# Performance work log

Measured on AMD Instinct MI355X. Metric: run time of the kernel, lower is better.

Reference implementation:

```python
import jax, jax.numpy as jnp
import numpy as np

BATCH, SEQ, IN_DIM, OUT_DIM = 8, 512, 32, 1
D_MODEL, N_LAYERS = 512, 4
D_INNER = 2 * D_MODEL          # expand_factor=2
D_STATE = 16
D_CONV = 4
DT_RANK = (D_MODEL + 15) // 16  # ceil(d_model/16) = 32


def setup_inputs() -> dict:
    key = jax.random.key(0)
    ks = iter(jax.random.split(key, 24))
    def w(shape, fan_in):
        return jax.random.normal(next(ks), shape, jnp.float32) * (fan_in ** -0.5)
    dt = jax.random.uniform(next(ks), (N_LAYERS, D_INNER), jnp.float32, 1e-3, 0.1)
    A_log = jnp.broadcast_to(jnp.log(jnp.arange(1, D_STATE + 1, dtype=jnp.float32)),
                             (N_LAYERS, D_INNER, D_STATE)) * 1.0
    return {
        "x": jax.random.normal(next(ks), (BATCH, SEQ, IN_DIM), jnp.float32),
        "enc_w": w((D_MODEL, IN_DIM), IN_DIM),
        "enc_b": jnp.zeros((D_MODEL,), jnp.float32),
        "in_proj_w": w((N_LAYERS, 2 * D_INNER, D_MODEL), D_MODEL),
        "conv_w": w((N_LAYERS, D_INNER, 1, D_CONV), D_CONV),
        "conv_b": jnp.zeros((N_LAYERS, D_INNER), jnp.float32),
        "x_proj_w": w((N_LAYERS, DT_RANK + 2 * D_STATE, D_INNER), D_INNER),
        "dt_proj_w": w((N_LAYERS, D_INNER, DT_RANK), DT_RANK),
        "dt_proj_b": jnp.log(jnp.expm1(dt)),  # inverse softplus init
        "A_log": A_log,
        "D": jnp.ones((N_LAYERS, D_INNER), jnp.float32),
        "out_proj_w": w((N_LAYERS, D_MODEL, D_INNER), D_INNER),
        "norm_w": jnp.ones((N_LAYERS, D_MODEL), jnp.float32),
        "dec_w1": w((D_MODEL // 2, D_MODEL), D_MODEL),
        "dec_b1": jnp.zeros((D_MODEL // 2,), jnp.float32),
        "dec_w2": w((OUT_DIM, D_MODEL // 2), D_MODEL // 2),
        "dec_b2": jnp.zeros((OUT_DIM,), jnp.float32),
    }


def _rmsnorm(x, w, eps=1e-5):
    return x * jax.lax.rsqrt(jnp.mean(x * x, axis=-1, keepdims=True) + eps) * w


def _mixer(x, in_w, cw, cb, xp_w, dtp_w, dtp_b, A_log, Dp, out_w):
    B, L, _ = x.shape
    xz = x @ in_w.T                               # (B,L,2*di)
    xr, z = jnp.split(xz, 2, axis=-1)
    # causal depthwise conv1d (cross-correlation, left pad d_conv-1)
    xc = jax.lax.conv_general_dilated(
        xr.transpose(0, 2, 1), cw, window_strides=(1,),
        padding=[(D_CONV - 1, 0)], feature_group_count=D_INNER,
        dimension_numbers=("NCW", "OIW", "NCW"))    # (B,di,L)
    xr = jax.nn.silu(xc.transpose(0, 2, 1) + cb)   # (B,L,di)
    dbc = xr @ xp_w.T                              # (B,L,dt_rank+2N)
    delta = jax.nn.softplus(dbc[..., :DT_RANK] @ dtp_w.T + dtp_b)  # (B,L,di)
    Bm = dbc[..., DT_RANK:DT_RANK + D_STATE]       # (B,L,N)
    Cm = dbc[..., DT_RANK + D_STATE:]              # (B,L,N)
    A = -jnp.exp(A_log)                            # (di,N)
    dA = jnp.exp(delta[..., None] * A)             # (B,L,di,N)
    dBx = delta[..., None] * Bm[:, :, None, :] * xr[..., None]
    def step(h, inputs):
        dA_t, dBx_t = inputs
        h = dA_t * h + dBx_t
        return h, h
    h0 = jnp.zeros((B, D_INNER, D_STATE), xr.dtype)
    _, hs = jax.lax.scan(step, h0, (dA.transpose(1, 0, 2, 3), dBx.transpose(1, 0, 2, 3)))
    y = jnp.einsum("lbdn,bln->bld", hs, Cm) + Dp * xr
    y = y * jax.nn.silu(z)
    return y @ out_w.T


def reference(x, enc_w, enc_b, in_proj_w, conv_w, conv_b, x_proj_w, dt_proj_w,
              dt_proj_b, A_log, D, out_proj_w, norm_w, dec_w1, dec_b1, dec_w2, dec_b2):
    h = x @ enc_w.T + enc_b
    for i in range(in_proj_w.shape[0]):   # residual pre-norm Mamba blocks
        h = h + _mixer(_rmsnorm(h, norm_w[i]), in_proj_w[i], conv_w[i], conv_b[i],
                       x_proj_w[i], dt_proj_w[i], dt_proj_b[i], A_log[i], D[i],
                       out_proj_w[i])
    h = h[:, -1, :]
    h = jax.nn.relu(h @ dec_w1.T + dec_b1)
    return (h @ dec_w2.T + dec_b2).reshape(-1)
```

## Files before the change

### kernel.cpp

```cpp
#include <hip/hip_runtime.h>
#include <math.h>

#define BATCH   8
#define SEQ     512
#define IN_DIM  32
#define D_MODEL 512
#define N_LAYERS 4
#define D_INNER 1024
#define D_STATE 16
#define D_CONV  4
#define DT_RANK 32
#define NTOK    (BATCH * SEQ)
#define BLK_T   32
#define NCHUNK  (SEQ / BLK_T)

typedef __attribute__((ext_vector_type(8))) short short8_t;
typedef __attribute__((ext_vector_type(4))) float floatx4;

__device__ __forceinline__ float sigmoidf_(float x) { return 1.f / (1.f + __expf(-x)); }

__device__ __forceinline__ unsigned short f2bf(float f) {
    unsigned int u = __float_as_uint(f);
    return (unsigned short)((u + 0x7fffu + ((u >> 16) & 1u)) >> 16);
}
__device__ __forceinline__ float bf2f(unsigned short u) {
    return __uint_as_float((unsigned int)u << 16);
}

__global__ __launch_bounds__(256) void cast_all_kernel(
    const float* __restrict__ a, unsigned short* __restrict__ oa, int qa,
    const float* __restrict__ b, unsigned short* __restrict__ ob, int qb,
    const float* __restrict__ c, unsigned short* __restrict__ oc, int qc)
{
    int v = blockIdx.x * 256 + threadIdx.x;
    const float* in; unsigned short* out;
    if (v < qa)                { in = a; out = oa; }
    else if (v < qa + qb)      { v -= qa; in = b; out = ob; }
    else if (v < qa + qb + qc) { v -= qa + qb; in = c; out = oc; }
    else return;
    const float4 x = *(const float4*)&in[v * 4];
    ushort4 o;
    o.x = f2bf(x.x); o.y = f2bf(x.y); o.z = f2bf(x.z); o.w = f2bf(x.w);
    *(ushort4*)&out[v * 4] = o;
}

template<int BM, int BN, bool OUTBF, bool ILV>
__global__ __launch_bounds__(256) void gemm_mfma(
    const unsigned short* __restrict__ A, int lda,
    const unsigned short* __restrict__ W, int ldw,
    const float* __restrict__ R,
    void* __restrict__ Cv, int ldc,
    int K)
{
    constexpr int MT = BM / 32;
    constexpr int NT = BN / 32;
    constexpr int SA = BM / 64;
    constexpr int SB = BN / 64;
    __shared__ __align__(16) unsigned short sA[BM * 32];
    __shared__ __align__(16) unsigned short sB[BN * 32];

    const int tid  = threadIdx.x;
    const int lane = tid & 63;
    const int wave = tid >> 6;
    const int wm0  = (wave >> 1) * (BM / 2);
    const int wn0  = (wave & 1) * (BN / 2);
    const int lrow = lane & 15;
    const int m0 = blockIdx.y * BM;
    const int n0 = blockIdx.x * BN;

    const unsigned short* aptr[SA];
    const unsigned short* bptr[SB];
    #pragma unroll
    for (int s = 0; s < SA; ++s) {
        const int r = wave * (BM / 4) + s * 16 + (lane >> 2);
        const int cc = (((lane & 3) ^ ((r >> 1) & 3))) * 8;
        aptr[s] = &A[(size_t)(m0 + r) * lda + cc];
    }
    #pragma unroll
    for (int s = 0; s < SB; ++s) {
        const int r = wave * (BN / 4) + s * 16 + (lane >> 2);
        const int cc = (((lane & 3) ^ ((r >> 1) & 3))) * 8;
        bptr[s] = &W[(size_t)(n0 + r) * ldw + cc];
    }
    int aoff[MT], boff[NT];
    #pragma unroll
    for (int mt = 0; mt < MT; ++mt) {
        const int m = wm0 + mt * 16 + lrow;
        aoff[mt] = m * 32 + (((lane >> 4) ^ ((m >> 1) & 3)) * 8);
    }
    #pragma unroll
    for (int nt = 0; nt < NT; ++nt) {
        const int n = wn0 + nt * 16 + lrow;
        boff[nt] = n * 32 + (((lane >> 4) ^ ((n >> 1) & 3)) * 8);
    }

    floatx4 acc[MT][NT];
    #pragma unroll
    for (int mt = 0; mt < MT; ++mt)
        #pragma unroll
        for (int nt = 0; nt < NT; ++nt)
            acc[mt][nt] = (floatx4){0.f, 0.f, 0.f, 0.f};

    for (int k0 = 0; k0 < K; k0 += 32) {
        #pragma unroll
        for (int s = 0; s < SA; ++s)
            __builtin_amdgcn_global_load_lds(
                (const __attribute__((address_space(1))) void*)(aptr[s] + k0),
                (__attribute__((address_space(3))) void*)&sA[(wave * (BM / 4) + s * 16) * 32],
                16, 0, 0);
        #pragma unroll
        for (int s = 0; s < SB; ++s)
            __builtin_amdgcn_global_load_lds(
                (const __attribute__((address_space(1))) void*)(bptr[s] + k0),
                (__attribute__((address_space(3))) void*)&sB[(wave * (BN / 4) + s * 16) * 32],
                16, 0, 0);
        __syncthreads();
        short8_t af[MT], bfr[NT];
        #pragma unroll
        for (int mt = 0; mt < MT; ++mt)
            af[mt] = *(const short8_t*)&sA[aoff[mt]];
        #pragma unroll
        for (int nt = 0; nt < NT; ++nt)
            bfr[nt] = *(const short8_t*)&sB[boff[nt]];
        #pragma unroll
        for (int mt = 0; mt < MT; ++mt)
            #pragma unroll
            for (int nt = 0; nt < NT; ++nt)
                acc[mt][nt] = __builtin_amdgcn_mfma_f32_16x16x32_bf16(af[mt], bfr[nt], acc[mt][nt], 0, 0, 0);
        __syncthreads();
    }

    #pragma unroll
    for (int mt = 0; mt < MT; ++mt) {
        const int mbase = m0 + wm0 + mt * 16 + (lane >> 4) * 4;
        #pragma unroll
        for (int nt = 0; nt < NT; ++nt) {
            const int n = n0 + wn0 + nt * 16 + (lane & 15);
            int np = n;
            if (ILV) np = (n < 32) ? n : ((n < 48) ? 32 + 2 * (n - 32) : 33 + 2 * (n - 48));
            #pragma unroll
            for (int r = 0; r < 4; ++r) {
                float v = acc[mt][nt][r];
                if (OUTBF) {
                    ((unsigned short*)Cv)[(size_t)(mbase + r) * ldc + np] = f2bf(v);
                } else {
                    if (R) v += R[(size_t)(mbase + r) * ldc + np];
                    ((float*)Cv)[(size_t)(mbase + r) * ldc + np] = v;
                }
            }
        }
    }
}

template<bool SOFTPLUS>
__global__ __launch_bounds__(256) void gemm_bt64(
    const float* __restrict__ A, int lda,
    const float* __restrict__ W,
    const float* __restrict__ bias,
    float* __restrict__ C,
    int N, int K, int ldc)
{
    __shared__ __align__(16) float As[16][64];
    __shared__ __align__(16) float Ws[16][64];
    const int tid = threadIdx.x;
    const int tx = tid & 15, ty = tid >> 4;
    const int m0 = blockIdx.y * 64, n0 = blockIdx.x * 64;
    const int lm = tid >> 2;
    const int lk = (tid & 3) * 4;

    float acc[4][4] = {};
    for (int k0 = 0; k0 < K; k0 += 16) {
        float4 av = *(const float4*)&A[(size_t)(m0 + lm) * lda + k0 + lk];
        float4 wv = *(const float4*)&W[(size_t)(n0 + lm) * K   + k0 + lk];
        As[lk + 0][lm] = av.x; As[lk + 1][lm] = av.y; As[lk + 2][lm] = av.z; As[lk + 3][lm] = av.w;
        Ws[lk + 0][lm] = wv.x; Ws[lk + 1][lm] = wv.y; Ws[lk + 2][lm] = wv.z; Ws[lk + 3][lm] = wv.w;
        __syncthreads();
        #pragma unroll
        for (int k = 0; k < 16; ++k) {
            float4 a4 = *(const float4*)&As[k][ty * 4];
            float4 b4 = *(const float4*)&Ws[k][tx * 4];
            float a[4] = {a4.x, a4.y, a4.z, a4.w};
            float b[4] = {b4.x, b4.y, b4.z, b4.w};
            #pragma unroll
            for (int i = 0; i < 4; ++i)
                #pragma unroll
                for (int j = 0; j < 4; ++j)
                    acc[i][j] = fmaf(a[i], b[j], acc[i][j]);
        }
        __syncthreads();
    }
    #pragma unroll
    for (int i = 0; i < 4; ++i) {
        const int m = m0 + ty * 4 + i;
        #pragma unroll
        for (int j = 0; j < 4; ++j) {
            const int n = n0 + tx * 4 + j;
            float v = acc[i][j] + bias[n];
            if (SOFTPLUS) v = (v > 20.f) ? v : log1pf(__expf(v));
            C[(size_t)m * ldc + n] = v;
        }
    }
}

__global__ __launch_bounds__(256) void rmsnorm_kernel(
    const float* __restrict__ h, const float* __restrict__ w, unsigned short* __restrict__ xn)
{
    const int tok = blockIdx.x, tid = threadIdx.x;
    const float* row = h + (size_t)tok * D_MODEL;
    float v0 = row[tid], v1 = row[tid + 256];
    float s = v0 * v0 + v1 * v1;
    #pragma unroll
    for (int off = 32; off > 0; off >>= 1) s += __shfl_down(s, off, 64);
    __shared__ float ss[4];
    if ((tid & 63) == 0) ss[tid >> 6] = s;
    __syncthreads();
    const float total = ss[0] + ss[1] + ss[2] + ss[3];
    const float scale = rsqrtf(total * (1.f / (float)D_MODEL) + 1e-5f);
    unsigned short* orow = xn + (size_t)tok * D_MODEL;
    orow[tid]       = f2bf(v0 * scale * w[tid]);
    orow[tid + 256] = f2bf(v1 * scale * w[tid + 256]);
}

__global__ __launch_bounds__(256) void conv_silu_kernel(
    const unsigned short* __restrict__ xz, const float* __restrict__ cw,
    const float* __restrict__ cb, unsigned short* __restrict__ xr_bf)
{
    const int idx = blockIdx.x * 256 + threadIdx.x;
    const int dq  = idx & (D_INNER / 8 - 1);
    const int d0  = dq * 8;
    const int tok = idx >> 7;
    const int l   = tok & (SEQ - 1);

    float4 w4[8];
    #pragma unroll
    for (int j = 0; j < 8; ++j) w4[j] = *(const float4*)&cw[(d0 + j) * 4];
    const float4 cb0 = *(const float4*)&cb[d0];
    const float4 cb1 = *(const float4*)&cb[d0 + 4];
    float acc[8] = {cb0.x, cb0.y, cb0.z, cb0.w, cb1.x, cb1.y, cb1.z, cb1.w};

    #pragma unroll
    for (int k = 0; k < D_CONV; ++k) {
        const int t = l - (D_CONV - 1) + k;
        if (t >= 0) {
            const short8_t xv = *(const short8_t*)&xz[(size_t)(tok + t - l) * (2 * D_INNER) + d0];
            #pragma unroll
            for (int j = 0; j < 8; ++j)
                acc[j] = fmaf(bf2f((unsigned short)xv[j]), ((const float*)&w4[j])[k], acc[j]);
        }
    }
    short8_t o;
    #pragma unroll
    for (int j = 0; j < 8; ++j) {
        const float v = acc[j] * sigmoidf_(acc[j]);
        o[j] = (short)f2bf(v);
    }
    *(short8_t*)&xr_bf[(size_t)tok * D_INNER + d0] = o;
}


__global__ __launch_bounds__(256) void scan_state4(
    const float* __restrict__ dbc, const unsigned short* __restrict__ xrbf,
    const float* __restrict__ delta, const float* __restrict__ A_log,
    float* __restrict__ hend, float* __restrict__ cdend)
{
    const int tid = threadIdx.x;
    const int l = tid & 63, s = tid >> 6;
    const int b = blockIdx.y, c = blockIdx.z;
    const int d = blockIdx.x * 64 + l;
    const int base0 = b * SEQ + c * BLK_T;

    float An4[4];
    #pragma unroll
    for (int j = 0; j < 4; ++j)
        An4[j] = -__expf(A_log[(size_t)d * D_STATE + 4 * s + j]);

    float h0 = 0.f, h1 = 0.f, h2 = 0.f, h3 = 0.f, cd = 0.f;

    float4 pb0A, pb1A, pb0B, pb1B;
    float dtA, dtB;
    unsigned short xA, xB;

    #define LD_ST(S0, S1, DT, X, T)                                               \
    {                                                                             \
        const int row = base0 + (T);                                              \
        const float4* r4 = (const float4*)&dbc[(size_t)row * 64 + 32 + 8 * s];    \
        S0 = r4[0]; S1 = r4[1];                                                   \
        DT = delta[(size_t)row * D_INNER + d];                                    \
        X  = xrbf[(size_t)row * D_INNER + d];                                     \
    }
    #define STEP_ST(S0, S1, DT, X)                                                \
    {                                                                             \
        const float xf = bf2f(X);                                                 \
        const float dx = DT * xf;                                                 \
        cd += DT;                                                                 \
        h0 = fmaf(__expf(DT * An4[0]), h0, dx * S0.x);                            \
        h1 = fmaf(__expf(DT * An4[1]), h1, dx * S0.z);                            \
        h2 = fmaf(__expf(DT * An4[2]), h2, dx * S1.x);                            \
        h3 = fmaf(__expf(DT * An4[3]), h3, dx * S1.z);                            \
    }

    LD_ST(pb0A, pb1A, dtA, xA, 0);
    for (int t = 0; t < BLK_T; t += 2) {
        LD_ST(pb0B, pb1B, dtB, xB, t + 1);
        STEP_ST(pb0A, pb1A, dtA, xA);
        if (t + 2 < BLK_T) LD_ST(pb0A, pb1A, dtA, xA, t + 2);
        STEP_ST(pb0B, pb1B, dtB, xB);
    }
    #undef LD_ST
    #undef STEP_ST

    const size_t cb = (size_t)b * NCHUNK + c;
    hend[(cb * D_STATE + 4 * s + 0) * D_INNER + d] = h0;
    hend[(cb * D_STATE + 4 * s + 1) * D_INNER + d] = h1;
    hend[(cb * D_STATE + 4 * s + 2) * D_INNER + d] = h2;
    hend[(cb * D_STATE + 4 * s + 3) * D_INNER + d] = h3;
    if (s == 0) cdend[cb * D_INNER + d] = cd;
}

__global__ __launch_bounds__(256) void scan_full16(
    const float* __restrict__ dbc, const unsigned short* __restrict__ xrbf,
    const unsigned short* __restrict__ xzbf, const float* __restrict__ delta,
    const float* __restrict__ A_log, const float* __restrict__ Dp,
    const float* __restrict__ hend, const float* __restrict__ cdend,
    unsigned short* __restrict__ y)
{
    const int tid = threadIdx.x;
    const int b = blockIdx.y, c = blockIdx.z;
    const int d = blockIdx.x * 256 + tid;
    const int base0 = b * SEQ + c * BLK_T;

    float An[16];
    {
        const float4* ar = (const float4*)&A_log[(size_t)d * D_STATE];
        #pragma unroll
        for (int q = 0; q < 4; ++q) {
            const float4 a4 = ar[q];
            An[4*q+0] = -__expf(a4.x); An[4*q+1] = -__expf(a4.y);
            An[4*q+2] = -__expf(a4.z); An[4*q+3] = -__expf(a4.w);
        }
    }
    const float Dd = Dp[d];

    float h[16];
    #pragma unroll
    for (int n = 0; n < 16; ++n) h[n] = 0.f;
    for (int cc = 0; cc < c; ++cc) {
        const size_t pb = (size_t)b * NCHUNK + cc;
        const float e = cdend[pb * D_INNER + d];
        #pragma unroll
        for (int n = 0; n < 16; ++n)
            h[n] = fmaf(__expf(e * An[n]), h[n], hend[(pb * D_STATE + n) * D_INNER + d]);
    }

    float4 bcA[8], bcB[8];
    float dtA, dtB;
    unsigned short xA, xB, zA, zB;

    #define LD_FU(BC, DT, X, Z, T)                                                \
    {                                                                             \
        const int row = base0 + (T);                                              \
        const float4* r4 = (const float4*)&dbc[(size_t)row * 64 + 32];            \
        _Pragma("unroll")                                                         \
        for (int q = 0; q < 8; ++q) BC[q] = r4[q];                                \
        DT = delta[(size_t)row * D_INNER + d];                                    \
        X  = xrbf[(size_t)row * D_INNER + d];                                     \
        Z  = xzbf[(size_t)row * (2 * D_INNER) + D_INNER + d];                     \
    }
    #define STEP_FU(BC, DT, X, Z, T)                                              \
    {                                                                             \
        const float xf = bf2f(X);                                                 \
        const float dx = DT * xf;                                                 \
        float p = 0.f;                                                            \
        _Pragma("unroll")                                                         \
        for (int q = 0; q < 8; ++q) {                                             \
            const float4 v = BC[q];                                               \
            const float e0 = __expf(DT * An[2*q]);                                \
            h[2*q]   = fmaf(e0, h[2*q],   dx * v.x);                              \
            p = fmaf(v.y, h[2*q], p);                                             \
            const float e1 = __expf(DT * An[2*q+1]);                              \
            h[2*q+1] = fmaf(e1, h[2*q+1], dx * v.z);                              \
            p = fmaf(v.w, h[2*q+1], p);                                           \
        }                                                                         \
        const float zf = bf2f(Z);                                                 \
        const float yv = fmaf(Dd, xf, p);                                         \
        y[(size_t)(base0 + (T)) * D_INNER + d] = f2bf(yv * zf * sigmoidf_(zf));   \
    }

    LD_FU(bcA, dtA, xA, zA, 0);
    for (int t = 0; t < BLK_T; t += 2) {
        LD_FU(bcB, dtB, xB, zB, t + 1);
        STEP_FU(bcA, dtA, xA, zA, t);
        if (t + 2 < BLK_T) LD_FU(bcA, dtA, xA, zA, t + 2);
        STEP_FU(bcB, dtB, xB, zB, t + 1);
    }
    #undef LD_FU
    #undef STEP_FU
}

__global__ __launch_bounds__(256) void dec_kernel(
    const float* __restrict__ h, const float* __restrict__ w1, const float* __restrict__ b1,
    const float* __restrict__ w2, const float* __restrict__ b2, float* __restrict__ out)
{
    __shared__ __align__(16) float hr[D_MODEL];
    __shared__ float part[4];
    const int b = blockIdx.x, j = threadIdx.x;
    const float* row = h + ((size_t)(b * SEQ + SEQ - 1)) * D_MODEL;
    hr[j] = row[j];
    hr[j + 256] = row[j + 256];
    __syncthreads();
    float acc = b1[j];
    const float* wr = w1 + (size_t)j * D_MODEL;
    for (int k = 0; k < D_MODEL; k += 4) {
        const float4 wvv = *(const float4*)&wr[k];
        const float4 hv = *(const float4*)&hr[k];
        acc = fmaf(wvv.x, hv.x, acc); acc = fmaf(wvv.y, hv.y, acc);
        acc = fmaf(wvv.z, hv.z, acc); acc = fmaf(wvv.w, hv.w, acc);
    }
    float s = fmaxf(acc, 0.f) * w2[j];
    #pragma unroll
    for (int off = 32; off > 0; off >>= 1) s += __shfl_down(s, off, 64);
    if ((j & 63) == 0) part[j >> 6] = s;
    __syncthreads();
    if (j == 0) out[b] = part[0] + part[1] + part[2] + part[3] + b2[0];
}

extern "C" void kernel_launch(void* const* d_in, const int* in_sizes, int n_in,
                              void* d_out, int out_size, void* d_ws, size_t ws_size,
                              hipStream_t stream)
{
    const float* x      = (const float*)d_in[0];
    const float* enc_w  = (const float*)d_in[1];
    const float* enc_b  = (const float*)d_in[2];
    const float* in_w   = (const float*)d_in[3];
    const float* conv_w = (const float*)d_in[4];
    const float* conv_b = (const float*)d_in[5];
    const float* xp_w   = (const float*)d_in[6];
    const float* dtp_w  = (const float*)d_in[7];
    const float* dtp_b  = (const float*)d_in[8];
    const float* A_log  = (const float*)d_in[9];
    const float* Dp     = (const float*)d_in[10];
    const float* out_w  = (const float*)d_in[11];
    const float* norm_w = (const float*)d_in[12];
    const float* dec_w1 = (const float*)d_in[13];
    const float* dec_b1 = (const float*)d_in[14];
    const float* dec_w2 = (const float*)d_in[15];
    const float* dec_b2 = (const float*)d_in[16];
    float* out = (float*)d_out;

    float* ws     = (float*)d_ws;
    float* h      = ws;
    float* dbc    = h + (size_t)NTOK * D_MODEL;
    float* delta  = dbc + (size_t)NTOK * 64;
    float* hendb  = delta + (size_t)NTOK * D_INNER;
    float* cdendb = hendb + (size_t)BATCH * NCHUNK * D_STATE * D_INNER;
    float* wsend  = cdendb + (size_t)BATCH * NCHUNK * D_INNER;
    unsigned short* xz_bf   = (unsigned short*)(wsend);
    unsigned short* xn_bf   = xz_bf   + (size_t)NTOK * 2 * D_INNER;
    unsigned short* y_bf    = xn_bf   + (size_t)NTOK * D_MODEL;
    unsigned short* xr_bf   = y_bf    + (size_t)NTOK * D_INNER;
    unsigned short* inw_bf  = xr_bf   + (size_t)NTOK * D_INNER;
    unsigned short* outw_bf = inw_bf  + (size_t)N_LAYERS * 2 * D_INNER * D_MODEL;
    unsigned short* xpw_bf  = outw_bf + (size_t)N_LAYERS * D_MODEL * D_INNER;

    const int qa = N_LAYERS * 2 * D_INNER * D_MODEL / 4;
    const int qb = N_LAYERS * D_MODEL * D_INNER / 4;
    const int qc = N_LAYERS * 64 * D_INNER / 4;
    cast_all_kernel<<<(qa + qb + qc + 255) / 256, 256, 0, stream>>>(
        in_w, inw_bf, qa, out_w, outw_bf, qb, xp_w, xpw_bf, qc);

    gemm_bt64<false><<<dim3(D_MODEL / 64, NTOK / 64), 256, 0, stream>>>(
        x, IN_DIM, enc_w, enc_b, h, D_MODEL, IN_DIM, D_MODEL);

    for (int i = 0; i < N_LAYERS; ++i) {
        rmsnorm_kernel<<<NTOK, 256, 0, stream>>>(h, norm_w + (size_t)i * D_MODEL, xn_bf);

        gemm_mfma<128, 128, true, false><<<dim3(2 * D_INNER / 128, NTOK / 128), 256, 0, stream>>>(
            xn_bf, D_MODEL, inw_bf + (size_t)i * 2 * D_INNER * D_MODEL, D_MODEL,
            nullptr, xz_bf, 2 * D_INNER, D_MODEL);

        conv_silu_kernel<<<NTOK * (D_INNER / 8) / 256, 256, 0, stream>>>(
            xz_bf, conv_w + (size_t)i * D_INNER * D_CONV, conv_b + (size_t)i * D_INNER, xr_bf);

        gemm_mfma<64, 64, false, true><<<dim3(1, NTOK / 64), 256, 0, stream>>>(
            xr_bf, D_INNER, xpw_bf + (size_t)i * 64 * D_INNER, D_INNER,
            nullptr, dbc, 64, D_INNER);

        gemm_bt64<true><<<dim3(D_INNER / 64, NTOK / 64), 256, 0, stream>>>(
            dbc, 64, dtp_w + (size_t)i * D_INNER * DT_RANK, dtp_b + (size_t)i * D_INNER,
            delta, D_INNER, DT_RANK, D_INNER);

        scan_state4<<<dim3(D_INNER / 64, BATCH, NCHUNK - 1), 256, 0, stream>>>(
            dbc, xr_bf, delta, A_log + (size_t)i * D_INNER * D_STATE,
            hendb, cdendb);

        scan_full16<<<dim3(D_INNER / 256, BATCH, NCHUNK), 256, 0, stream>>>(
            dbc, xr_bf, xz_bf, delta,
            A_log + (size_t)i * D_INNER * D_STATE, Dp + (size_t)i * D_INNER,
            hendb, cdendb, y_bf);

        gemm_mfma<64, 64, false, false><<<dim3(D_MODEL / 64, NTOK / 64), 256, 0, stream>>>(
            y_bf, D_INNER, outw_bf + (size_t)i * D_MODEL * D_INNER, D_INNER,
            h, h, D_MODEL, D_INNER);
    }

    dec_kernel<<<BATCH, 256, 0, stream>>>(h, dec_w1, dec_b1, dec_w2, dec_b2, out);
}
```

Before: 698.8 us.

## Split-K the x_proj GEMM and fuse partial reduction with dt_proj softplus

The x_proj GEMM (N=64, K=1024) previously launched only 64 blocks. It is now split four ways along K into separate partial buffers, which gives 256 blocks. A new kernel sums the four partials and writes dbc with the interleaved B/C column layout that the ILV epilogue used to produce. The same kernel then computes the dt_proj projection plus bias and softplus directly, replacing the separate gemm_bt64 launch. The cost is extra partial-buffer traffic and workspace, and the dt_proj work now runs as scalar FMAs in a kernel with 8 rows per block.

```diff
diff --git a/kernel.cpp b/kernel.cpp
--- a/kernel.cpp
+++ b/kernel.cpp
@@ -44,7 +44,7 @@
     *(ushort4*)&out[v * 4] = o;
 }
 
-template<int BM, int BN, bool OUTBF, bool ILV>
+template<int BM, int BN, bool OUTBF, bool ILV, int KSPLIT = 1>
 __global__ __launch_bounds__(256) void gemm_mfma(
     const unsigned short* __restrict__ A, int lda,
     const unsigned short* __restrict__ W, int ldw,
@@ -58,6 +58,13 @@
     constexpr int SB = BN / 64;
     __shared__ __align__(16) unsigned short sA[BM * 32];
     __shared__ __align__(16) unsigned short sB[BN * 32];
+
+    if (KSPLIT > 1) {
+        const int kz = blockIdx.z;
+        A += (size_t)kz * K;
+        W += (size_t)kz * K;
+        Cv = (void*)((float*)Cv + (size_t)kz * NTOK * ldc);
+    }
 
     const int tid  = threadIdx.x;
     const int lane = tid & 63;
@@ -255,6 +262,55 @@
         o[j] = (short)f2bf(v);
     }
     *(short8_t*)&xr_bf[(size_t)tok * D_INNER + d0] = o;
+}
+
+#define RD_ROWS 8
+__global__ __launch_bounds__(256) void reduce_delta_kernel(
+    const float* __restrict__ part,
+    const float* __restrict__ dtp_w, const float* __restrict__ dtp_b,
+    float* __restrict__ dbc, float* __restrict__ delta)
+{
+    __shared__ float sdt[RD_ROWS][DT_RANK];
+    const int tid = threadIdx.x;
+    const int r0 = blockIdx.x * RD_ROWS;
+
+    #pragma unroll
+    for (int it = 0; it < RD_ROWS * 64 / 256; ++it) {
+        const int u = it * 256 + tid;
+        const int row = u >> 6, col = u & 63;
+        const size_t idx = (size_t)(r0 + row) * 64 + col;
+        const float s = part[idx] + part[idx + (size_t)NTOK * 64]
+                      + part[idx + 2 * (size_t)NTOK * 64] + part[idx + 3 * (size_t)NTOK * 64];
+        if (col < DT_RANK) sdt[row][col] = s;
+        const int np = (col < 32) ? col : ((col < 48) ? 32 + 2 * (col - 32) : 33 + 2 * (col - 48));
+        dbc[(size_t)(r0 + row) * 64 + np] = s;
+    }
+    __syncthreads();
+
+    #pragma unroll
+    for (int dd = 0; dd < D_INNER / 256; ++dd) {
+        const int d = dd * 256 + tid;
+        float4 wv[8];
+        {
+            const float4* wr = (const float4*)&dtp_w[(size_t)d * DT_RANK];
+            #pragma unroll
+            for (int q = 0; q < 8; ++q) wv[q] = wr[q];
+        }
+        const float bb = dtp_b[d];
+        #pragma unroll
+        for (int row = 0; row < RD_ROWS; ++row) {
+            float a = bb;
+            #pragma unroll
+            for (int q = 0; q < 8; ++q) {
+                a = fmaf(sdt[row][4 * q + 0], wv[q].x, a);
+                a = fmaf(sdt[row][4 * q + 1], wv[q].y, a);
+                a = fmaf(sdt[row][4 * q + 2], wv[q].z, a);
+                a = fmaf(sdt[row][4 * q + 3], wv[q].w, a);
+            }
+            a = (a > 20.f) ? a : log1pf(__expf(a));
+            delta[(size_t)(r0 + row) * D_INNER + d] = a;
+        }
+    }
 }
 
 
@@ -453,7 +509,8 @@
     float* delta  = dbc + (size_t)NTOK * 64;
     float* hendb  = delta + (size_t)NTOK * D_INNER;
     float* cdendb = hendb + (size_t)BATCH * NCHUNK * D_STATE * D_INNER;
-    float* wsend  = cdendb + (size_t)BATCH * NCHUNK * D_INNER;
+    float* xpart  = cdendb + (size_t)BATCH * NCHUNK * D_INNER;
+    float* wsend  = xpart + (size_t)4 * NTOK * 64;
     unsigned short* xz_bf   = (unsigned short*)(wsend);
     unsigned short* xn_bf   = xz_bf   + (size_t)NTOK * 2 * D_INNER;
     unsigned short* y_bf    = xn_bf   + (size_t)NTOK * D_MODEL;
@@ -481,13 +538,13 @@
         conv_silu_kernel<<<NTOK * (D_INNER / 8) / 256, 256, 0, stream>>>(
             xz_bf, conv_w + (size_t)i * D_INNER * D_CONV, conv_b + (size_t)i * D_INNER, xr_bf);
 
-        gemm_mfma<64, 64, false, true><<<dim3(1, NTOK / 64), 256, 0, stream>>>(
+        gemm_mfma<64, 64, false, false, 4><<<dim3(1, NTOK / 64, 4), 256, 0, stream>>>(
             xr_bf, D_INNER, xpw_bf + (size_t)i * 64 * D_INNER, D_INNER,
-            nullptr, dbc, 64, D_INNER);
-
-        gemm_bt64<true><<<dim3(D_INNER / 64, NTOK / 64), 256, 0, stream>>>(
-            dbc, 64, dtp_w + (size_t)i * D_INNER * DT_RANK, dtp_b + (size_t)i * D_INNER,
-            delta, D_INNER, DT_RANK, D_INNER);
+            nullptr, xpart, 64, D_INNER / 4);
+
+        reduce_delta_kernel<<<NTOK / RD_ROWS, 256, 0, stream>>>(
+            xpart, dtp_w + (size_t)i * D_INNER * DT_RANK, dtp_b + (size_t)i * D_INNER,
+            dbc, delta);
 
         scan_state4<<<dim3(D_INNER / 64, BATCH, NCHUNK - 1), 256, 0, stream>>>(
             dbc, xr_bf, delta, A_log + (size_t)i * D_INNER * D_STATE,
```

After: 675.6 us. -3.3%, faster.
